# Kernel optimization log

Measured on AMD Instinct MI355X. Metric: run time of the kernel, lower is better.

Reference implementation:

```python
import jax, jax.numpy as jnp
import numpy as np

MARGIN = 1.0
EPS = 1e-6  # F.pairwise_distance adds eps to the elementwise diff


def setup_inputs() -> dict:
    key = jax.random.key(0)
    k1, k2, k3 = jax.random.split(key, 3)
    N, D = 8192, 64
    anchor_embeddings = jax.random.normal(k1, (N, D), dtype=jnp.float32)
    positive_embeddings = jax.random.normal(k2, (N, D), dtype=jnp.float32)
    labels = jax.random.randint(k3, (N,), 0, 2, dtype=jnp.int64)
    return {
        "anchor_embeddings": anchor_embeddings,
        "positive_embeddings": positive_embeddings,
        "labels": labels,
    }


def _pairwise_dist(a, p):
    # dist[i, j] = ||(a_i + eps) - p_j||_2, matching F.pairwise_distance's
    # norm(x1 - x2 + eps). Computed via the Gram trick to avoid an [N,N,D]
    # intermediate.
    a = a + EPS
    a2 = jnp.sum(a * a, axis=-1)                      # [N]
    p2 = jnp.sum(p * p, axis=-1)                      # [N]
    sq = a2[:, None] + p2[None, :] - 2.0 * (a @ p.T)  # [N, N]
    return jnp.sqrt(jnp.maximum(sq, 1e-12))


def reference(anchor_embeddings, positive_embeddings, labels):
    N = anchor_embeddings.shape[0]
    dist = _pairwise_dist(anchor_embeddings, positive_embeddings)  # [N, N]
    pos_dist = jnp.diagonal(dist)                                  # [N], d(a_i, p_i)
    hinge = jax.nn.relu(pos_dist[:, None] - dist + MARGIN)         # [N, N]
    # pair (i, j) contributes iff labels[i] == 1 and i != j
    row_mask = (labels == 1)[:, None]
    offdiag = ~jnp.eye(N, dtype=bool)
    mask = (row_mask & offdiag).astype(hinge.dtype)
    count = jnp.sum(mask)
    total = jnp.sum(hinge * mask)
    return jnp.where(count > 0, total / jnp.maximum(count, 1.0), 0.0)
```

## Files before the change

kernel.cpp:

```cpp
#include <hip/hip_runtime.h>
#include <hip/hip_bf16.h>

#define NROWS 8192
#define DDIM 64
#define MARGIN_F 1.0f
#define EPS_F 1e-6f


typedef __attribute__((ext_vector_type(8))) short bf16x8;
typedef __attribute__((ext_vector_type(4))) float f32x4;

static __device__ __forceinline__ unsigned short f2bf(float x) {
    __hip_bfloat16 h = __float2bfloat16(x);
    return *reinterpret_cast<unsigned short*>(&h);
}
static __device__ __forceinline__ float bf2f(unsigned short u) {
    return __uint_as_float(((unsigned)u) << 16);
}

__global__ __launch_bounds__(256) void
prep_compact_kernel(const float* __restrict__ A, const float* __restrict__ P,
                    const int* __restrict__ labels,
                    unsigned short* __restrict__ Abf, unsigned short* __restrict__ Pbf,
                    float* __restrict__ a2g, float* __restrict__ pdg,
                    float* __restrict__ p2g, float* __restrict__ hdg,
                    int* __restrict__ sel, int* __restrict__ cnt) {
    __shared__ int lab[256 * 33];
    __shared__ int scan[256];
    int t = threadIdx.x;

    if (blockIdx.x < 512) {
        int gid = blockIdx.x * 256 + t;
        int row = gid >> 4;
        int c4  = (gid & 15) * 4;
        float4 a = *(const float4*)&A[row * DDIM + c4];
        float4 p = *(const float4*)&P[row * DDIM + c4];
        a.x += EPS_F; a.y += EPS_F; a.z += EPS_F; a.w += EPS_F;
        ushort4 ab, pb;
        ab.x = f2bf(a.x); ab.y = f2bf(a.y); ab.z = f2bf(a.z); ab.w = f2bf(a.w);
        pb.x = f2bf(p.x); pb.y = f2bf(p.y); pb.z = f2bf(p.z); pb.w = f2bf(p.w);
        *(ushort4*)&Abf[row * DDIM + c4] = ab;
        *(ushort4*)&Pbf[row * DDIM + c4] = pb;
        float va2 = a.x*a.x + a.y*a.y + a.z*a.z + a.w*a.w;
        float vp2 = p.x*p.x + p.y*p.y + p.z*p.z + p.w*p.w;
        float vap = a.x*p.x + a.y*p.y + a.z*p.z + a.w*p.w;
        float vdd = bf2f(ab.x)*bf2f(pb.x) + bf2f(ab.y)*bf2f(pb.y)
                  + bf2f(ab.z)*bf2f(pb.z) + bf2f(ab.w)*bf2f(pb.w);
        #pragma unroll
        for (int off = 8; off; off >>= 1) {
            va2 += __shfl_xor(va2, off);
            vp2 += __shfl_xor(vp2, off);
            vap += __shfl_xor(vap, off);
            vdd += __shfl_xor(vdd, off);
        }
        if ((t & 15) == 0) {
            a2g[row] = va2;
            p2g[row] = vp2;
            float pd = sqrtf(fmaxf(va2 + vp2 - 2.0f * vap, 1e-12f)) + MARGIN_F;
            pdg[row] = pd;
            float sqd = fmaxf(va2 + vp2 - 2.0f * vdd, 1e-12f);
            hdg[row] = fmaxf(pd - __builtin_amdgcn_sqrtf(sqd), 0.0f);
        }
    } else {
        #pragma unroll
        for (int i = 0; i < 32; ++i) {
            int j = i * 256 + t;
            lab[(j >> 5) * 33 + (j & 31)] = labels[j];
        }
        __syncthreads();
        int lc = 0;
        #pragma unroll
        for (int i = 0; i < 32; ++i) lc += (lab[t * 33 + i] == 1) ? 1 : 0;
        scan[t] = lc;
        __syncthreads();
        for (int off = 1; off < 256; off <<= 1) {
            int v = (t >= off) ? scan[t - off] : 0;
            __syncthreads();
            if (t >= off) scan[t] += v;
            __syncthreads();
        }
        int o = scan[t] - lc;
        for (int i = 0; i < 32; ++i) {
            if (lab[t * 33 + i] == 1) sel[o++] = t * 32 + i;
        }
        if (t == 255) *cnt = scan[255];
    }
}

__global__ __launch_bounds__(256) void
main_kernel(const unsigned short* __restrict__ Abf, const unsigned short* __restrict__ Pbf,
            const float* __restrict__ a2g, const float* __restrict__ pdg,
            const float* __restrict__ p2g, const int* __restrict__ sel,
            const int* __restrict__ cnt, float* __restrict__ partial) {
    __shared__ float sA2[128], sPd[128], sP2[128];
    __shared__ int   sGi[128];
    __shared__ float wsum[4];

    int M = *cnt;
    int row0 = blockIdx.y << 7;
    int col0 = blockIdx.x << 7;
    int bid  = (blockIdx.y << 6) + blockIdx.x;
    int t = threadIdx.x;
    if (row0 >= M) { if (t == 0) partial[bid] = 0.0f; return; }

    int wid  = t >> 6;
    int lane = t & 63;
    int wm   = (wid >> 1) << 6;
    int wn   = (wid & 1) << 6;
    int lm   = lane & 15;
    int quad = lane >> 4;

    bf16x8 bg[2][4];
    #pragma unroll
    for (int b = 0; b < 4; ++b) {
        const unsigned short* pb = Pbf + (size_t)(col0 + wn + b * 16 + lm) * DDIM + quad * 8;
        bg[0][b] = *(const bf16x8*)pb;
        bg[1][b] = *(const bf16x8*)(pb + 32);
    }

    if (t < 128) {
        int gi = sel[min(row0 + t, M - 1)];
        sGi[t] = gi;
        sA2[t] = a2g[gi];
        sPd[t] = pdg[gi];
        sP2[t] = p2g[col0 + t];
    }
    __syncthreads();

    bf16x8 af[2][4];
    #pragma unroll
    for (int a = 0; a < 4; ++a) {
        const unsigned short* pa = Abf + (size_t)sGi[wm + a * 16 + lm] * DDIM + quad * 8;
        af[0][a] = *(const bf16x8*)pa;
        af[1][a] = *(const bf16x8*)(pa + 32);
    }

    f32x4 acc[4][4] = {};
    #pragma unroll
    for (int s = 0; s < 2; ++s)
        #pragma unroll
        for (int a = 0; a < 4; ++a)
            #pragma unroll
            for (int b = 0; b < 4; ++b)
                acc[a][b] = __builtin_amdgcn_mfma_f32_16x16x32_bf16(af[s][a], bg[s][b], acc[a][b], 0, 0, 0);

    float spv[4];
    #pragma unroll
    for (int b = 0; b < 4; ++b) spv[b] = sP2[wn + b * 16 + lm];

    float bsum = 0.0f;
    #pragma unroll
    for (int a = 0; a < 4; ++a) {
        #pragma unroll
        for (int r = 0; r < 4; ++r) {
            int il = wm + a * 16 + quad * 4 + r;
            float rm  = ((row0 + il) < M) ? 1.0f : 0.0f;
            float ra2 = sA2[il];
            float rpd = sPd[il];
            #pragma unroll
            for (int b = 0; b < 4; ++b) {
                float sq = fmaf(-2.0f, acc[a][b][r], ra2 + spv[b]);
                float h  = rpd - __builtin_amdgcn_sqrtf(sq);
                bsum = fmaf(fmaxf(h, 0.0f), rm, bsum);
            }
        }
    }

    #pragma unroll
    for (int off = 32; off; off >>= 1) bsum += __shfl_xor(bsum, off);
    if (lane == 0) wsum[wid] = bsum;
    __syncthreads();
    if (t == 0) partial[bid] = wsum[0] + wsum[1] + wsum[2] + wsum[3];
}

__global__ __launch_bounds__(256) void
finalize_kernel(const int* __restrict__ cnt, const float* __restrict__ partial,
                const float* __restrict__ hdg, const int* __restrict__ sel,
                float* __restrict__ out) {
    __shared__ float wsum[4];
    int t = threadIdx.x;
    const float4* p4 = (const float4*)partial;
    float s = 0.0f;
    #pragma unroll
    for (int i = 0; i < 4; ++i) {
        float4 v = p4[i * 256 + t];
        s += v.x + v.y + v.z + v.w;
    }
    int M = *cnt;
    for (int idx = t; idx < M; idx += 256) s -= hdg[sel[idx]];
    #pragma unroll
    for (int off = 32; off; off >>= 1) s += __shfl_xor(s, off);
    if ((t & 63) == 0) wsum[t >> 6] = s;
    __syncthreads();
    if (t == 0) {
        float tot = wsum[0] + wsum[1] + wsum[2] + wsum[3];
        float c = (float)M * (float)(NROWS - 1);
        out[0] = (M > 0) ? tot / c : 0.0f;
    }
}

extern "C" void kernel_launch(void* const* d_in, const int* in_sizes, int n_in,
                              void* d_out, int out_size, void* d_ws, size_t ws_size,
                              hipStream_t stream) {
    const float* A      = (const float*)d_in[0];
    const float* P      = (const float*)d_in[1];
    const int*   labels = (const int*)d_in[2];
    float* out = (float*)d_out;

    char* ws = (char*)d_ws;
    unsigned short* Abf = (unsigned short*)(ws);
    unsigned short* Pbf = (unsigned short*)(ws + (1 << 20));
    float* a2g     = (float*)(ws + (2 << 20));
    float* pdg     = (float*)(ws + (2 << 20) + 32768);
    float* p2g     = (float*)(ws + (2 << 20) + 65536);
    int*   sel     = (int*)(ws + (2 << 20) + 98304);
    int*   cnt     = (int*)(ws + (2 << 20) + 131072);
    float* partial = (float*)(ws + (2 << 20) + 135168);
    float* hdg     = (float*)(ws + (2 << 20) + 151552);

    prep_compact_kernel<<<dim3(513), dim3(256), 0, stream>>>(A, P, labels, Abf, Pbf,
                                                             a2g, pdg, p2g, hdg, sel, cnt);

    dim3 grid(NROWS / 128, NROWS / 128);
    main_kernel<<<grid, dim3(256), 0, stream>>>(Abf, Pbf, a2g, pdg, p2g, sel, cnt, partial);

    finalize_kernel<<<1, dim3(256), 0, stream>>>(cnt, partial, hdg, sel, out);
}
```

Before: 92.71 us.

## Fuse finalize into main kernel via last-block reduction and shrink grid

Removes the separate finalize launch: each main-kernel block atomically bumps a done counter, and the last block to finish sums the partials and the diagonal correction. The grid shrinks from 64x64 to 64x34 blocks, which loop over row tiles so early-exit blocks are no longer launched for unselected rows. The label-compaction scan now uses wave shuffles instead of a barrier-heavy shared-memory scan. In exchange it adds atomics and a serialized tail reduction in one block, and each block loops over row tiles, which can leave it imbalanced when M is near 4096.

```diff
diff --git a/kernel.cpp b/kernel.cpp
--- a/kernel.cpp
+++ b/kernel.cpp
@@ -5,6 +5,8 @@
 #define DDIM 64
 #define MARGIN_F 1.0f
 #define EPS_F 1e-6f
+#define GRID_Y 34
+#define NBLK (64 * GRID_Y)
 
 
 typedef __attribute__((ext_vector_type(8))) short bf16x8;
@@ -24,9 +26,8 @@
                     unsigned short* __restrict__ Abf, unsigned short* __restrict__ Pbf,
                     float* __restrict__ a2g, float* __restrict__ pdg,
                     float* __restrict__ p2g, float* __restrict__ hdg,
-                    int* __restrict__ sel, int* __restrict__ cnt) {
-    __shared__ int lab[256 * 33];
-    __shared__ int scan[256];
+                    int* __restrict__ sel, int* __restrict__ cnt,
+                    unsigned int* __restrict__ done) {
     int t = threadIdx.x;
 
     if (blockIdx.x < 512) {
@@ -62,6 +63,8 @@
             hdg[row] = fmaxf(pd - __builtin_amdgcn_sqrtf(sqd), 0.0f);
         }
     } else {
+        __shared__ int lab[256 * 33];
+        __shared__ int wtot[4];
         #pragma unroll
         for (int i = 0; i < 32; ++i) {
             int j = i * 256 + t;
@@ -71,19 +74,23 @@
         int lc = 0;
         #pragma unroll
         for (int i = 0; i < 32; ++i) lc += (lab[t * 33 + i] == 1) ? 1 : 0;
-        scan[t] = lc;
-        __syncthreads();
-        for (int off = 1; off < 256; off <<= 1) {
-            int v = (t >= off) ? scan[t - off] : 0;
-            __syncthreads();
-            if (t >= off) scan[t] += v;
-            __syncthreads();
-        }
-        int o = scan[t] - lc;
+        int lane = t & 63, wid = t >> 6;
+        int sc = lc;
+        #pragma unroll
+        for (int off = 1; off < 64; off <<= 1) {
+            int v = __shfl_up(sc, off);
+            if (lane >= off) sc += v;
+        }
+        if (lane == 63) wtot[wid] = sc;
+        __syncthreads();
+        int wpre = 0;
+        #pragma unroll
+        for (int w = 0; w < 4; ++w) wpre += (w < wid) ? wtot[w] : 0;
+        int o = wpre + sc - lc;
         for (int i = 0; i < 32; ++i) {
             if (lab[t * 33 + i] == 1) sel[o++] = t * 32 + i;
         }
-        if (t == 255) *cnt = scan[255];
+        if (t == 255) { *cnt = wpre + sc; *done = 0u; }
     }
 }
 
@@ -91,24 +98,22 @@
 main_kernel(const unsigned short* __restrict__ Abf, const unsigned short* __restrict__ Pbf,
             const float* __restrict__ a2g, const float* __restrict__ pdg,
             const float* __restrict__ p2g, const int* __restrict__ sel,
-            const int* __restrict__ cnt, float* __restrict__ partial) {
+            const int* __restrict__ cnt, float* __restrict__ partial,
+            const float* __restrict__ hdg, unsigned int* __restrict__ done,
+            float* __restrict__ out) {
     __shared__ float sA2[128], sPd[128], sP2[128];
     __shared__ int   sGi[128];
     __shared__ float wsum[4];
-
-    int M = *cnt;
-    int row0 = blockIdx.y << 7;
-    int col0 = blockIdx.x << 7;
-    int bid  = (blockIdx.y << 6) + blockIdx.x;
+    __shared__ int   lastFlag;
+
     int t = threadIdx.x;
-    if (row0 >= M) { if (t == 0) partial[bid] = 0.0f; return; }
-
     int wid  = t >> 6;
     int lane = t & 63;
     int wm   = (wid >> 1) << 6;
     int wn   = (wid & 1) << 6;
     int lm   = lane & 15;
     int quad = lane >> 4;
+    int col0 = blockIdx.x << 7;
 
     bf16x8 bg[2][4];
     #pragma unroll
@@ -117,51 +122,58 @@
         bg[0][b] = *(const bf16x8*)pb;
         bg[1][b] = *(const bf16x8*)(pb + 32);
     }
-
-    if (t < 128) {
-        int gi = sel[min(row0 + t, M - 1)];
-        sGi[t] = gi;
-        sA2[t] = a2g[gi];
-        sPd[t] = pdg[gi];
-        sP2[t] = p2g[col0 + t];
-    }
-    __syncthreads();
-
-    bf16x8 af[2][4];
-    #pragma unroll
-    for (int a = 0; a < 4; ++a) {
-        const unsigned short* pa = Abf + (size_t)sGi[wm + a * 16 + lm] * DDIM + quad * 8;
-        af[0][a] = *(const bf16x8*)pa;
-        af[1][a] = *(const bf16x8*)(pa + 32);
-    }
-
-    f32x4 acc[4][4] = {};
-    #pragma unroll
-    for (int s = 0; s < 2; ++s)
-        #pragma unroll
-        for (int a = 0; a < 4; ++a)
+    if (t < 128) sP2[t] = p2g[col0 + t];
+
+    int M = *cnt;
+    int ntiles = (M + 127) >> 7;
+
+    float bsum = 0.0f;
+    for (int rt = blockIdx.y; rt < ntiles; rt += GRID_Y) {
+        int row0 = rt << 7;
+        __syncthreads();
+        if (t < 128) {
+            int gi = sel[min(row0 + t, M - 1)];
+            sGi[t] = gi;
+            sA2[t] = a2g[gi];
+            sPd[t] = pdg[gi];
+        }
+        __syncthreads();
+
+        bf16x8 af[2][4];
+        #pragma unroll
+        for (int a = 0; a < 4; ++a) {
+            const unsigned short* pa = Abf + (size_t)sGi[wm + a * 16 + lm] * DDIM + quad * 8;
+            af[0][a] = *(const bf16x8*)pa;
+            af[1][a] = *(const bf16x8*)(pa + 32);
+        }
+
+        f32x4 acc[4][4] = {};
+        #pragma unroll
+        for (int s = 0; s < 2; ++s)
             #pragma unroll
-            for (int b = 0; b < 4; ++b)
-                acc[a][b] = __builtin_amdgcn_mfma_f32_16x16x32_bf16(af[s][a], bg[s][b], acc[a][b], 0, 0, 0);
-
-    float spv[4];
-    #pragma unroll
-    for (int b = 0; b < 4; ++b) spv[b] = sP2[wn + b * 16 + lm];
-
-    float bsum = 0.0f;
-    #pragma unroll
-    for (int a = 0; a < 4; ++a) {
-        #pragma unroll
-        for (int r = 0; r < 4; ++r) {
-            int il = wm + a * 16 + quad * 4 + r;
-            float rm  = ((row0 + il) < M) ? 1.0f : 0.0f;
-            float ra2 = sA2[il];
-            float rpd = sPd[il];
+            for (int a = 0; a < 4; ++a)
+                #pragma unroll
+                for (int b = 0; b < 4; ++b)
+                    acc[a][b] = __builtin_amdgcn_mfma_f32_16x16x32_bf16(af[s][a], bg[s][b], acc[a][b], 0, 0, 0);
+
+        float spv[4];
+        #pragma unroll
+        for (int b = 0; b < 4; ++b) spv[b] = sP2[wn + b * 16 + lm];
+
+        #pragma unroll
+        for (int a = 0; a < 4; ++a) {
             #pragma unroll
-            for (int b = 0; b < 4; ++b) {
-                float sq = fmaf(-2.0f, acc[a][b][r], ra2 + spv[b]);
-                float h  = rpd - __builtin_amdgcn_sqrtf(sq);
-                bsum = fmaf(fmaxf(h, 0.0f), rm, bsum);
+            for (int r = 0; r < 4; ++r) {
+                int il = wm + a * 16 + quad * 4 + r;
+                float rm  = ((row0 + il) < M) ? 1.0f : 0.0f;
+                float ra2 = sA2[il];
+                float rpd = sPd[il];
+                #pragma unroll
+                for (int b = 0; b < 4; ++b) {
+                    float sq = fmaf(-2.0f, acc[a][b][r], ra2 + spv[b]);
+                    float h  = rpd - __builtin_amdgcn_sqrtf(sq);
+                    bsum = fmaf(fmaxf(h, 0.0f), rm, bsum);
+                }
             }
         }
     }
@@ -170,27 +182,30 @@
     for (int off = 32; off; off >>= 1) bsum += __shfl_xor(bsum, off);
     if (lane == 0) wsum[wid] = bsum;
     __syncthreads();
-    if (t == 0) partial[bid] = wsum[0] + wsum[1] + wsum[2] + wsum[3];
-}
-
-__global__ __launch_bounds__(256) void
-finalize_kernel(const int* __restrict__ cnt, const float* __restrict__ partial,
-                const float* __restrict__ hdg, const int* __restrict__ sel,
-                float* __restrict__ out) {
-    __shared__ float wsum[4];
-    int t = threadIdx.x;
-    const float4* p4 = (const float4*)partial;
+
+    int bid = blockIdx.y * 64 + blockIdx.x;
+    if (t == 0) {
+        float v = wsum[0] + wsum[1] + wsum[2] + wsum[3];
+        __hip_atomic_store(&partial[bid], v, __ATOMIC_RELAXED, __HIP_MEMORY_SCOPE_AGENT);
+        unsigned old = __hip_atomic_fetch_add(done, 1u, __ATOMIC_ACQ_REL, __HIP_MEMORY_SCOPE_AGENT);
+        lastFlag = (old == (unsigned)(NBLK - 1)) ? 1 : 0;
+    }
+    __syncthreads();
+    if (lastFlag == 0) return;
+
     float s = 0.0f;
-    #pragma unroll
-    for (int i = 0; i < 4; ++i) {
-        float4 v = p4[i * 256 + t];
-        s += v.x + v.y + v.z + v.w;
-    }
-    int M = *cnt;
+    for (int g = t; g < NBLK / 4; g += 256) {
+        int b0 = g * 4;
+        float x0 = __hip_atomic_load(&partial[b0 + 0], __ATOMIC_RELAXED, __HIP_MEMORY_SCOPE_AGENT);
+        float x1 = __hip_atomic_load(&partial[b0 + 1], __ATOMIC_RELAXED, __HIP_MEMORY_SCOPE_AGENT);
+        float x2 = __hip_atomic_load(&partial[b0 + 2], __ATOMIC_RELAXED, __HIP_MEMORY_SCOPE_AGENT);
+        float x3 = __hip_atomic_load(&partial[b0 + 3], __ATOMIC_RELAXED, __HIP_MEMORY_SCOPE_AGENT);
+        s += ((x0 + x1) + x2) + x3;
+    }
     for (int idx = t; idx < M; idx += 256) s -= hdg[sel[idx]];
     #pragma unroll
     for (int off = 32; off; off >>= 1) s += __shfl_xor(s, off);
-    if ((t & 63) == 0) wsum[t >> 6] = s;
+    if (lane == 0) wsum[wid] = s;
     __syncthreads();
     if (t == 0) {
         float tot = wsum[0] + wsum[1] + wsum[2] + wsum[3];
@@ -215,14 +230,13 @@
     float* p2g     = (float*)(ws + (2 << 20) + 65536);
     int*   sel     = (int*)(ws + (2 << 20) + 98304);
     int*   cnt     = (int*)(ws + (2 << 20) + 131072);
+    unsigned int* done = (unsigned int*)(ws + (2 << 20) + 131076);
     float* partial = (float*)(ws + (2 << 20) + 135168);
     float* hdg     = (float*)(ws + (2 << 20) + 151552);
 
     prep_compact_kernel<<<dim3(513), dim3(256), 0, stream>>>(A, P, labels, Abf, Pbf,
-                                                             a2g, pdg, p2g, hdg, sel, cnt);
-
-    dim3 grid(NROWS / 128, NROWS / 128);
-    main_kernel<<<grid, dim3(256), 0, stream>>>(Abf, Pbf, a2g, pdg, p2g, sel, cnt, partial);
-
-    finalize_kernel<<<1, dim3(256), 0, stream>>>(cnt, partial, hdg, sel, out);
-}
+                                                             a2g, pdg, p2g, hdg, sel, cnt, done);
+
+    main_kernel<<<dim3(64, GRID_Y), dim3(256), 0, stream>>>(Abf, Pbf, a2g, pdg, p2g, sel, cnt,
+                                                            partial, hdg, done, out);
+}
```

Result: slower. 120.4 us (+29.9%).
